# Performance work log

Hardware: AMD Instinct MI355X
Metric: run time of the kernel (lower is better)

The kernel has to match this reference:

```python
import jax, jax.numpy as jnp
import numpy as np

B, T, C = 4, 2048, 1024
H, DH = 16, 64  # num_heads, head_size; H*DH == C


def setup_inputs() -> dict:
    key = jax.random.key(0)
    ks = jax.random.split(key, 6)
    s = C ** -0.5
    x = jax.random.normal(ks[0], (B, T, C), dtype=jnp.float32)
    # per-head projection weights, stacked: [H, C, DH]
    Wq = jax.random.normal(ks[1], (H, C, DH), dtype=jnp.float32) * s
    Wk = jax.random.normal(ks[2], (H, C, DH), dtype=jnp.float32) * s
    Wv = jax.random.normal(ks[3], (H, C, DH), dtype=jnp.float32) * s
    # output projection (with bias, as nn.Linear default)
    Wo = jax.random.normal(ks[4], (C, C), dtype=jnp.float32) * s
    bo = jax.random.normal(ks[5], (C,), dtype=jnp.float32) * 0.01
    return {"x": x, "Wq": Wq, "Wk": Wk, "Wv": Wv, "Wo": Wo, "bo": bo}


def reference(x, Wq, Wk, Wv, Wo, bo):
    Bv, Tv, Cv = x.shape
    scale = DH ** -0.5
    # project to per-head q/k/v: [B, H, T, DH]
    q = jnp.einsum('btc,hcd->bhtd', x, Wq)
    k = jnp.einsum('btc,hcd->bhtd', x, Wk)
    v = jnp.einsum('btc,hcd->bhtd', x, Wv)
    # scaled scores [B, H, T, T] with causal mask
    scores = jnp.einsum('bhtd,bhsd->bhts', q, k) * scale
    causal = jnp.tril(jnp.ones((Tv, Tv), dtype=bool))
    scores = jnp.where(causal, scores, -jnp.inf)
    wei = jax.nn.softmax(scores, axis=-1)
    out = jnp.einsum('bhts,bhsd->bhtd', wei, v)
    # concat heads: [B, T, H*DH] == [B, T, C]
    out = out.transpose(0, 2, 1, 3).reshape(Bv, Tv, Cv)
    return out @ Wo.T + bo
```

## Files before the change

### kernel.cpp

```cpp
#include <hip/hip_runtime.h>
#include <stdint.h>

typedef unsigned short u16;
typedef __attribute__((ext_vector_type(8))) short short8;
typedef __attribute__((ext_vector_type(4))) float floatx4;

#define MFMA_BF16 __builtin_amdgcn_mfma_f32_16x16x32_bf16

#define BB 4
#define TT 2048
#define CC 1024
#define HH 16
#define DH 64
#define MM (BB * TT)
#define NQKV (3 * CC)

__device__ __forceinline__ u16 f2bf(float f) {
  union { float f; uint32_t u; } un;
  un.f = f;
  uint32_t u = un.u;
  u += 0x7fffu + ((u >> 16) & 1u);
  return (u16)(u >> 16);
}

__device__ __forceinline__ uint32_t pk2(float a, float b) {
  return (uint32_t)f2bf(a) | ((uint32_t)f2bf(b) << 16);
}

__device__ __forceinline__ uint32_t pktrunc(float a, float b) {
  union { float f; uint32_t u; } ua, ub;
  ua.f = a; ub.f = b;
  return __builtin_amdgcn_perm(ub.u, ua.u, 0x07060302u);
}

__device__ __forceinline__ void gload_lds16(const u16* g, u16* l) {
  __builtin_amdgcn_global_load_lds(
      (const __attribute__((address_space(1))) unsigned int*)g,
      (__attribute__((address_space(3))) unsigned int*)l, 16, 0, 0);
}

__global__ __launch_bounds__(256) void convert_kernel(
    const float* __restrict__ x, const float* __restrict__ Wq,
    const float* __restrict__ Wk, const float* __restrict__ Wv,
    const float* __restrict__ Wo, u16* __restrict__ xb,
    u16* __restrict__ Wt, u16* __restrict__ Wob) {
  __shared__ float T[32][33];
  int bid = blockIdx.x, tid = threadIdx.x;
  if (bid < 8192) {
    int i = (bid * 256 + tid) * 4;
    float4 f = *(const float4*)(x + i);
    uint2 o = {pk2(f.x, f.y), pk2(f.z, f.w)};
    *(uint2*)(xb + i) = o;
  } else if (bid < 8192 + 3072) {
    int tb = bid - 8192;
    int sec = tb >> 10, rem = tb & 1023;
    int h = rem >> 6, sub = rem & 63, ct = sub >> 1, dt = sub & 1;
    const float* W = (sec == 0) ? Wq : (sec == 1) ? Wk : Wv;
    int tx = tid & 31, ty = tid >> 5;
#pragma unroll
    for (int p = 0; p < 4; ++p)
      T[ty + 8 * p][tx] =
          W[((size_t)h * CC + ct * 32 + ty + 8 * p) * DH + dt * 32 + tx];
    __syncthreads();
#pragma unroll
    for (int p = 0; p < 4; ++p) {
      int n = sec * 1024 + h * 64 + dt * 32 + ty + 8 * p;
      Wt[(size_t)n * CC + ct * 32 + tx] = f2bf(T[tx][ty + 8 * p]);
    }
  } else {
    int i = ((bid - 11264) * 256 + tid) * 4;
    float4 f = *(const float4*)(Wo + i);
    uint2 o = {pk2(f.x, f.y), pk2(f.z, f.w)};
    *(uint2*)(Wob + i) = o;
  }
}

__global__ __launch_bounds__(512, 2) void gemm_qkv(
    const u16* __restrict__ A, const u16* __restrict__ Bt,
    u16* __restrict__ qout, u16* __restrict__ kout, u16* __restrict__ vout) {
  __shared__ u16 As[2 * 256 * 32];
  __shared__ u16 Bs[2 * 384 * 32];

  int tid = threadIdx.x;
  int lane = tid & 63, w = tid >> 6;
  int wr = w >> 2, wc = w & 3;
  int g = lane >> 4, c = lane & 15;
  int m0 = blockIdx.y * 256, n0 = blockIdx.x * 384;

  floatx4 acc[8][6];
#pragma unroll
  for (int i = 0; i < 8; ++i)
#pragma unroll
    for (int j = 0; j < 6; ++j) acc[i][j] = (floatx4){0.f, 0.f, 0.f, 0.f};

  int arow = tid >> 2, acol = (tid & 3) * 8;
  const u16* Ag = A + (size_t)(m0 + arow) * CC + acol;
  const u16* Bg = Bt + (size_t)(n0 + arow) * CC + acol;
  u16* asd = As + tid * 8;
  u16* bsd = Bs + tid * 8;

  const u16* Asr = As + (wr * 128 + c) * 32 + g * 8;
  const u16* Bsr = Bs + (wc * 96 + c) * 32 + g * 8;

  gload_lds16(Ag, asd);
  gload_lds16(Ag + (size_t)128 * CC, asd + 4096);
  gload_lds16(Bg, bsd);
  gload_lds16(Bg + (size_t)128 * CC, bsd + 4096);
  gload_lds16(Bg + (size_t)256 * CC, bsd + 8192);
  asm volatile("s_waitcnt vmcnt(0)" ::: "memory");
  __builtin_amdgcn_s_barrier();
  asm volatile("" ::: "memory");

#define GEMM_ITER(p, t)                                                       \
  {                                                                           \
    if ((t) + 1 < 32) {    \
      size_t ko = (size_t)((t) + 1) * 32;                                     \
      gload_lds16(Ag + ko, asd + ((p) ^ 1) * 8192);                           \
      gload_lds16(Ag + ko + (size_t)128 * CC, asd + ((p) ^ 1) * 8192 + 4096); \
      gload_lds16(Bg + ko, bsd + ((p) ^ 1) * 12288);                          \
      gload_lds16(Bg + ko + (size_t)128 * CC, bsd + ((p) ^ 1) * 12288 + 4096);\
      gload_lds16(Bg + ko + (size_t)256 * CC, bsd + ((p) ^ 1) * 12288 + 8192);\
    }                                                                         \
    short8 bfr[6];                                                            \
    _Pragma("unroll") for (int nt = 0; nt < 6; ++nt)                          \
        bfr[nt] = *(const short8*)(Bsr + (p) * 12288 + nt * 512);             \
    __builtin_amdgcn_s_setprio(1);                                            \
    _Pragma("unroll") for (int mt = 0; mt < 8; ++mt) {                        \
      short8 af = *(const short8*)(Asr + (p) * 8192 + mt * 512);              \
      _Pragma("unroll") for (int nt = 0; nt < 6; ++nt)                        \
          acc[mt][nt] = MFMA_BF16(af, bfr[nt], acc[mt][nt], 0, 0, 0);         \
    }                                                                         \
    __builtin_amdgcn_s_setprio(0);                                            \
    asm volatile("s_waitcnt vmcnt(0)" ::: "memory");    \
    __builtin_amdgcn_s_barrier();                                             \
    asm volatile("" ::: "memory");                                            \
  }

#pragma unroll 1
  for (int tt = 0; tt < 16; ++tt) {
    GEMM_ITER(0, 2 * tt);
    GEMM_ITER(1, 2 * tt + 1);
  }
#undef GEMM_ITER

  int mrow = m0 + wr * 128 + g * 4;
  int ncol = n0 + wc * 96 + c;
#pragma unroll
  for (int nt = 0; nt < 6; ++nt) {
    int n = ncol + nt * 16;
    int sec = n >> 10, h = (n >> 6) & 15, d = n & 63;
    u16* dst = (sec == 0) ? qout : (sec == 1) ? kout : vout;
    float sc = (sec == 0) ? 0.18033688011112042f : 1.f;
#pragma unroll
    for (int mt = 0; mt < 8; ++mt) {
#pragma unroll
      for (int r = 0; r < 4; ++r) {
        int m = mrow + mt * 16 + r;
        int b = m >> 11, t = m & 2047;
        dst[(((size_t)(b * HH + h)) * TT + t) * DH + d] =
            f2bf(acc[mt][nt][r] * sc);
      }
    }
  }
}

template <int MODE>
__global__ __launch_bounds__(256) void gemm_bt(
    const u16* __restrict__ A, const u16* __restrict__ Bt, int M, int N, int K,
    u16* __restrict__ qout, u16* __restrict__ kout, u16* __restrict__ vout,
    float* __restrict__ out, const float* __restrict__ bias) {
  __shared__ u16 As[128][64];
  __shared__ u16 Bs[128][64];
  int tid = threadIdx.x;
  int lane = tid & 63, w = tid >> 6;
  int wm = w >> 1, wn = w & 1;
  int g = lane >> 4, c = lane & 15;
  int m0 = blockIdx.y * 128, n0 = blockIdx.x * 128;

  floatx4 acc[4][4];
#pragma unroll
  for (int i = 0; i < 4; ++i)
#pragma unroll
    for (int j = 0; j < 4; ++j) acc[i][j] = (floatx4){0.f, 0.f, 0.f, 0.f};

  int srow = 32 * w + (lane >> 3);
  int scol = (lane & 7) * 8;
  const u16* Ag = A + (size_t)(m0 + srow) * K + scol;
  const u16* Bg = Bt + (size_t)(n0 + srow) * K + scol;
  u16* AsB = &As[32 * w][0];
  u16* BsB = &Bs[32 * w][0];

  for (int k0 = 0; k0 < K; k0 += 64) {
    __syncthreads();
#pragma unroll
    for (int j = 0; j < 4; ++j)
      gload_lds16(Ag + k0 + (size_t)j * 8 * K, AsB + j * 512);
#pragma unroll
    for (int j = 0; j < 4; ++j)
      gload_lds16(Bg + k0 + (size_t)j * 8 * K, BsB + j * 512);
    __syncthreads();
#pragma unroll
    for (int kc = 0; kc < 2; ++kc) {
      short8 af[4], bfv[4];
#pragma unroll
      for (int mt = 0; mt < 4; ++mt)
        af[mt] = *(const short8*)(&As[wm * 64 + mt * 16 + c][kc * 32 + g * 8]);
#pragma unroll
      for (int nt = 0; nt < 4; ++nt)
        bfv[nt] = *(const short8*)(&Bs[wn * 64 + nt * 16 + c][kc * 32 + g * 8]);
#pragma unroll
      for (int mt = 0; mt < 4; ++mt)
#pragma unroll
        for (int nt = 0; nt < 4; ++nt)
          acc[mt][nt] = MFMA_BF16(af[mt], bfv[nt], acc[mt][nt], 0, 0, 0);
    }
  }

#pragma unroll
  for (int mt = 0; mt < 4; ++mt) {
#pragma unroll
    for (int nt = 0; nt < 4; ++nt) {
#pragma unroll
      for (int r = 0; r < 4; ++r) {
        int m = m0 + wm * 64 + mt * 16 + g * 4 + r;
        int n = n0 + wn * 64 + nt * 16 + c;
        float v = acc[mt][nt][r];
        if (MODE == 0) {
          int b = m >> 11, t = m & 2047;
          int sec = n >> 10, h = (n >> 6) & 15, d = n & 63;
          size_t idx = (((size_t)(b * HH + h)) * TT + t) * DH + d;
          if (sec == 0)
            qout[idx] = f2bf(v * 0.18033688011112042f);
          else if (sec == 1)
            kout[idx] = f2bf(v);
          else
            vout[idx] = f2bf(v);
        } else {
          out[(size_t)m * N + n] = v + bias[n];
        }
      }
    }
  }
}

__global__ __launch_bounds__(256) void vtrans(const u16* __restrict__ v,
                                              u16* __restrict__ vP) {
  __shared__ u16 Ld[64][72];
  int tile = blockIdx.x, bh = blockIdx.y, tid = threadIdx.x;
  int row = tid >> 2, col = (tid & 3) * 16;
  const u16* src = v + ((size_t)bh * TT + tile * 64 + row) * DH + col;
  *(uint4*)(&Ld[row][col]) = *(const uint4*)(src);
  *(uint4*)(&Ld[row][col + 8]) = *(const uint4*)(src + 8);
  __syncthreads();
  int d = tid >> 2, u0 = (tid & 3) * 16;
  union { u16 h[16]; uint4 q[2]; } o;
#pragma unroll
  for (int k = 0; k < 16; ++k) {
    int u = u0 + k;
    int s = ((u & 3) << 4) | (u >> 2);
    o.h[k] = Ld[s][d];
  }
  u16* dst = vP + ((size_t)(bh * DH + d)) * TT + tile * 64 + u0;
  *(uint4*)(dst) = o.q[0];
  *(uint4*)(dst + 8) = o.q[1];
}

__constant__ unsigned char CHUNK_X[24] = {15, 15, 7, 14, 14, 13, 13, 6,
                                          12, 12, 11, 11, 5, 10, 10, 9,
                                          9,  4,  8,  8,  3, 2,  1,  0};
__constant__ unsigned char CHUNK_H[24] = {0, 1, 2, 0, 1, 0, 1, 2, 0, 1, 0, 1,
                                          2, 0, 1, 0, 1, 2, 0, 1, 2, 2, 2, 2};

__global__ __launch_bounds__(256, 4) void flash_attn(
    const u16* __restrict__ q, const u16* __restrict__ k,
    const u16* __restrict__ vP, u16* __restrict__ O,
    float* __restrict__ opart, float* __restrict__ lpart) {
  __shared__ u16 Ks[64][72];
  __shared__ u16 Vs[64][72];
  __shared__ u16 Ps[4][32][72];

  int tid = threadIdx.x;
  int lane = tid & 63, w = tid >> 6;
  int g = lane >> 4, c = lane & 15;

  int id = blockIdx.x;
  int e = id >> 6, bh = id & 63;
  int x = CHUNK_X[e], hf = CHUNK_H[e];
  int sb, se;
  if (hf == 2) {
    sb = 0; se = 2 * x + 2;
  } else {
    int n = x + 1; sb = hf * n; se = sb + n;
  }
  int t0 = x << 7;

  const u16* qb = q + (size_t)bh * TT * DH;
  const u16* kb = k + (size_t)bh * TT * DH;
  const u16* vb = vP + (size_t)bh * DH * TT;

  short8 qf[2][2];
#pragma unroll
  for (int mt = 0; mt < 2; ++mt) {
    int qrow = t0 + w * 32 + mt * 16 + c;
#pragma unroll
    for (int kc = 0; kc < 2; ++kc)
      qf[mt][kc] = *(const short8*)(qb + (size_t)qrow * DH + kc * 32 + g * 8);
  }

  const floatx4 zf = {0.f, 0.f, 0.f, 0.f};
  const short8 onesf = {(short)0x3F80, (short)0x3F80, (short)0x3F80,
                        (short)0x3F80, (short)0x3F80, (short)0x3F80,
                        (short)0x3F80, (short)0x3F80};

  floatx4 oacc[2][4];
#pragma unroll
  for (int mt = 0; mt < 2; ++mt)
#pragma unroll
    for (int nt = 0; nt < 4; ++nt) oacc[mt][nt] = zf;
  floatx4 lacc[2];
  lacc[0] = zf;
  lacc[1] = zf;

  int srow = tid >> 2, scol = (tid & 3) * 16;
  const u16* kbase = kb + (size_t)srow * DH + scol;
  const u16* vbase = vb + (size_t)srow * TT + scol;

  uint4 kr0 = *(const uint4*)(kbase + (size_t)(sb << 6) * DH);
  uint4 kr1 = *(const uint4*)(kbase + (size_t)(sb << 6) * DH + 8);
  uint4 vr0 = *(const uint4*)(vbase + (sb << 6));
  uint4 vr1 = *(const uint4*)(vbase + (sb << 6) + 8);

  int nfull = 2 * x;
  int wmax = t0 + w * 32 + 31;
  for (int it = sb; it < se; ++it) {
    int s0 = it << 6;
    __syncthreads();
    *(uint4*)(&Ks[srow][scol]) = kr0;
    *(uint4*)(&Ks[srow][scol + 8]) = kr1;
    *(uint4*)(&Vs[srow][scol]) = vr0;
    *(uint4*)(&Vs[srow][scol + 8]) = vr1;
    __syncthreads();
    if (it + 1 < se) {
      size_t koff = (size_t)((it + 1) << 6) * DH;
      int voff = (it + 1) << 6;
      kr0 = *(const uint4*)(kbase + koff);
      kr1 = *(const uint4*)(kbase + koff + 8);
      vr0 = *(const uint4*)(vbase + voff);
      vr1 = *(const uint4*)(vbase + voff + 8);
    }
    if (s0 > wmax) continue;
    bool masked = (it >= nfull);

    floatx4 z[2][4];
#pragma unroll
    for (int n = 0; n < 4; ++n) {
      short8 kf = *(const short8*)(&Ks[n * 16 + c][g * 8]);
      z[0][n] = MFMA_BF16(qf[0][0], kf, zf, 0, 0, 0);
      z[1][n] = MFMA_BF16(qf[1][0], kf, zf, 0, 0, 0);
    }
#pragma unroll
    for (int n = 0; n < 4; ++n) {
      short8 kf = *(const short8*)(&Ks[n * 16 + c][32 + g * 8]);
      z[0][n] = MFMA_BF16(qf[0][1], kf, z[0][n], 0, 0, 0);
      z[1][n] = MFMA_BF16(qf[1][1], kf, z[1][n], 0, 0, 0);
    }

#pragma unroll
    for (int mt = 0; mt < 2; ++mt) {
      int qr = t0 + w * 32 + mt * 16 + g * 4;
#pragma unroll
      for (int r = 0; r < 4; ++r) {
        float p0 = exp2f(z[mt][0][r]);
        float p1 = exp2f(z[mt][1][r]);
        float p2 = exp2f(z[mt][2][r]);
        float p3 = exp2f(z[mt][3][r]);
        if (masked) {
          if (s0 + c > qr + r) p0 = 0.f;
          if (s0 + 16 + c > qr + r) p1 = 0.f;
          if (s0 + 32 + c > qr + r) p2 = 0.f;
          if (s0 + 48 + c > qr + r) p3 = 0.f;
        }
        uint2 pk = {pktrunc(p0, p1), pktrunc(p2, p3)};
        *(uint2*)(&Ps[w][mt * 16 + g * 4 + r][4 * c]) = pk;
      }
    }

#pragma unroll
    for (int kc = 0; kc < 2; ++kc) {
      short8 pf0 = *(const short8*)(&Ps[w][c][kc * 32 + g * 8]);
      short8 pf1 = *(const short8*)(&Ps[w][16 + c][kc * 32 + g * 8]);
      lacc[0] = MFMA_BF16(pf0, onesf, lacc[0], 0, 0, 0);
      lacc[1] = MFMA_BF16(pf1, onesf, lacc[1], 0, 0, 0);
#pragma unroll
      for (int nt = 0; nt < 4; ++nt) {
        short8 vf = *(const short8*)(&Vs[nt * 16 + c][kc * 32 + g * 8]);
        oacc[0][nt] = MFMA_BF16(pf0, vf, oacc[0][nt], 0, 0, 0);
        oacc[1][nt] = MFMA_BF16(pf1, vf, oacc[1][nt], 0, 0, 0);
      }
    }
  }

  int b = bh >> 4, h = bh & 15;
  if (hf == 2) {
#pragma unroll
    for (int mt = 0; mt < 2; ++mt) {
      float inv[4];
#pragma unroll
      for (int r = 0; r < 4; ++r) inv[r] = 1.f / lacc[mt][r];
#pragma unroll
      for (int nt = 0; nt < 4; ++nt)
#pragma unroll
        for (int r = 0; r < 4; ++r) {
          int trow = t0 + w * 32 + mt * 16 + g * 4 + r;
          O[((size_t)b * TT + trow) * CC + h * DH + nt * 16 + c] =
              f2bf(oacc[mt][nt][r] * inv[r]);
        }
    }
  } else {
    float* os = opart + ((size_t)hf * 65536 + (size_t)bh * 1024) * 64;
    float* ls = lpart + (size_t)hf * 65536 + (size_t)bh * 1024;
#pragma unroll
    for (int mt = 0; mt < 2; ++mt) {
      int r0 = t0 - 1024 + w * 32 + mt * 16 + g * 4;
#pragma unroll
      for (int nt = 0; nt < 4; ++nt)
#pragma unroll
        for (int r = 0; r < 4; ++r)
          os[(size_t)(r0 + r) * 64 + nt * 16 + c] = oacc[mt][nt][r];
      if (c == 0)
#pragma unroll
        for (int r = 0; r < 4; ++r) ls[r0 + r] = lacc[mt][r];
    }
  }
}

__global__ __launch_bounds__(256) void merge_heavy(
    const float* __restrict__ op, const float* __restrict__ lp,
    u16* __restrict__ O) {
  int gid = blockIdx.x * 256 + threadIdx.x;
  int dq = gid & 15;
  int row = gid >> 4;
  float4 a = *(const float4*)(op + (size_t)row * 64 + dq * 4);
  float4 b = *(const float4*)(op + ((size_t)row + 65536) * 64 + dq * 4);
  float inv = 1.f / (lp[row] + lp[row + 65536]);
  int bh = row >> 10, lr = row & 1023;
  int bb = bh >> 4, h = bh & 15;
  u16* dst = O + ((size_t)bb * TT + 1024 + lr) * CC + h * DH + dq * 4;
  uint2 o = {pk2((a.x + b.x) * inv, (a.y + b.y) * inv),
             pk2((a.z + b.z) * inv, (a.w + b.w) * inv)};
  *(uint2*)dst = o;
}

extern "C" void kernel_launch(void* const* d_in, const int* in_sizes, int n_in,
                              void* d_out, int out_size, void* d_ws,
                              size_t ws_size, hipStream_t stream) {
  const float* x = (const float*)d_in[0];
  const float* Wq = (const float*)d_in[1];
  const float* Wk = (const float*)d_in[2];
  const float* Wv = (const float*)d_in[3];
  const float* Wo = (const float*)d_in[4];
  const float* bo = (const float*)d_in[5];
  float* out = (float*)d_out;

  u16* ws = (u16*)d_ws;
  u16* xb = ws;
  u16* Wt = xb + 8388608;
  u16* Wob = Wt + 3145728;
  u16* qw = Wob + 1048576;
  u16* kw = qw + 8388608;
  u16* vw = kw + 8388608;
  u16* vP = vw + 8388608;
  u16* Ow = xb;
  float* opart = (float*)d_out;
  float* lpart = (float*)Wt;

  convert_kernel<<<12288, 256, 0, stream>>>(x, Wq, Wk, Wv, Wo, xb, Wt, Wob);

  gemm_qkv<<<dim3(NQKV / 384, MM / 256), 512, 0, stream>>>(
      xb, Wt, qw, kw, vw);

  vtrans<<<dim3(TT / 64, BB * HH), 256, 0, stream>>>(vw, vP);

  flash_attn<<<dim3(1536), 256, 0, stream>>>(qw, kw, vP, Ow, opart, lpart);

  merge_heavy<<<dim3(4096), 256, 0, stream>>>(opart, lpart, Ow);

  gemm_bt<1><<<dim3(CC / 128, MM / 128), 256, 0, stream>>>(
      Ow, Wob, MM, CC, CC, nullptr, nullptr, nullptr, out, bo);
}
```

Measured before the change: 281.0 us.

## Restructure QKV GEMM into 128-row tiles with triple-buffered split-phase pipeline

```diff
diff --git a/kernel.cpp b/kernel.cpp
--- a/kernel.cpp
+++ b/kernel.cpp
@@ -37,6 +37,12 @@
   __builtin_amdgcn_global_load_lds(
       (const __attribute__((address_space(1))) unsigned int*)g,
       (__attribute__((address_space(3))) unsigned int*)l, 16, 0, 0);
+}
+
+__device__ __forceinline__ void BAR() {
+  asm volatile("" ::: "memory");
+  __builtin_amdgcn_s_barrier();
+  asm volatile("" ::: "memory");
 }
 
 __global__ __launch_bounds__(256) void convert_kernel(
@@ -78,18 +84,18 @@
 __global__ __launch_bounds__(512, 2) void gemm_qkv(
     const u16* __restrict__ A, const u16* __restrict__ Bt,
     u16* __restrict__ qout, u16* __restrict__ kout, u16* __restrict__ vout) {
-  __shared__ u16 As[2 * 256 * 32];
-  __shared__ u16 Bs[2 * 384 * 32];
+  __shared__ u16 As[3 * 128 * 32];
+  __shared__ u16 Bs[3 * 384 * 32];
 
   int tid = threadIdx.x;
   int lane = tid & 63, w = tid >> 6;
   int wr = w >> 2, wc = w & 3;
   int g = lane >> 4, c = lane & 15;
-  int m0 = blockIdx.y * 256, n0 = blockIdx.x * 384;
-
-  floatx4 acc[8][6];
-#pragma unroll
-  for (int i = 0; i < 8; ++i)
+  int m0 = blockIdx.y * 128, n0 = blockIdx.x * 384;
+
+  floatx4 acc[4][6];
+#pragma unroll
+  for (int i = 0; i < 4; ++i)
 #pragma unroll
     for (int j = 0; j < 6; ++j) acc[i][j] = (floatx4){0.f, 0.f, 0.f, 0.f};
 
@@ -99,51 +105,96 @@
   u16* asd = As + tid * 8;
   u16* bsd = Bs + tid * 8;
 
-  const u16* Asr = As + (wr * 128 + c) * 32 + g * 8;
-  const u16* Bsr = Bs + (wc * 96 + c) * 32 + g * 8;
+  int aro = (wr * 64 + c) * 32 + g * 8;
+  int bro = (wc * 96 + c) * 32 + g * 8;
 
   gload_lds16(Ag, asd);
-  gload_lds16(Ag + (size_t)128 * CC, asd + 4096);
   gload_lds16(Bg, bsd);
   gload_lds16(Bg + (size_t)128 * CC, bsd + 4096);
   gload_lds16(Bg + (size_t)256 * CC, bsd + 8192);
-  asm volatile("s_waitcnt vmcnt(0)" ::: "memory");
-  __builtin_amdgcn_s_barrier();
-  asm volatile("" ::: "memory");
-
-#define GEMM_ITER(p, t)                                                       \
+  gload_lds16(Ag + 32, asd + 4096);
+  gload_lds16(Bg + 32, bsd + 12288);
+  gload_lds16(Bg + 32 + (size_t)128 * CC, bsd + 12288 + 4096);
+  gload_lds16(Bg + 32 + (size_t)256 * CC, bsd + 12288 + 8192);
+  asm volatile("s_waitcnt vmcnt(4)" ::: "memory");
+  BAR();
+
+#define QTILE(SCA, SCB, SPA, SPB, T2, STG, VMW)                               \
   {                                                                           \
-    if ((t) + 1 < 32) {    \
-      size_t ko = (size_t)((t) + 1) * 32;                                     \
-      gload_lds16(Ag + ko, asd + ((p) ^ 1) * 8192);                           \
-      gload_lds16(Ag + ko + (size_t)128 * CC, asd + ((p) ^ 1) * 8192 + 4096); \
-      gload_lds16(Bg + ko, bsd + ((p) ^ 1) * 12288);                          \
-      gload_lds16(Bg + ko + (size_t)128 * CC, bsd + ((p) ^ 1) * 12288 + 4096);\
-      gload_lds16(Bg + ko + (size_t)256 * CC, bsd + ((p) ^ 1) * 12288 + 8192);\
+    short8 af0 = *(const short8*)(As + (SCA) + aro);                          \
+    short8 af1 = *(const short8*)(As + (SCA) + aro + 512);                    \
+    short8 af2 = *(const short8*)(As + (SCA) + aro + 1024);                   \
+    short8 af3 = *(const short8*)(As + (SCA) + aro + 1536);                   \
+    short8 bv0 = *(const short8*)(Bs + (SCB) + bro);                          \
+    short8 bv1 = *(const short8*)(Bs + (SCB) + bro + 512);                    \
+    short8 bv2 = *(const short8*)(Bs + (SCB) + bro + 1024);                   \
+    if (STG) {                                                                \
+      gload_lds16(Ag + (size_t)(T2) * 32, asd + (SPA));                       \
+      gload_lds16(Bg + (size_t)(T2) * 32, bsd + (SPB));                       \
     }                                                                         \
-    short8 bfr[6];                                                            \
-    _Pragma("unroll") for (int nt = 0; nt < 6; ++nt)                          \
-        bfr[nt] = *(const short8*)(Bsr + (p) * 12288 + nt * 512);             \
+    BAR();                                                                    \
     __builtin_amdgcn_s_setprio(1);                                            \
-    _Pragma("unroll") for (int mt = 0; mt < 8; ++mt) {                        \
-      short8 af = *(const short8*)(Asr + (p) * 8192 + mt * 512);              \
-      _Pragma("unroll") for (int nt = 0; nt < 6; ++nt)                        \
-          acc[mt][nt] = MFMA_BF16(af, bfr[nt], acc[mt][nt], 0, 0, 0);         \
+    acc[0][0] = MFMA_BF16(af0, bv0, acc[0][0], 0, 0, 0);                      \
+    acc[0][1] = MFMA_BF16(af0, bv1, acc[0][1], 0, 0, 0);                      \
+    acc[0][2] = MFMA_BF16(af0, bv2, acc[0][2], 0, 0, 0);                      \
+    acc[1][0] = MFMA_BF16(af1, bv0, acc[1][0], 0, 0, 0);                      \
+    acc[1][1] = MFMA_BF16(af1, bv1, acc[1][1], 0, 0, 0);                      \
+    acc[1][2] = MFMA_BF16(af1, bv2, acc[1][2], 0, 0, 0);                      \
+    acc[2][0] = MFMA_BF16(af2, bv0, acc[2][0], 0, 0, 0);                      \
+    acc[2][1] = MFMA_BF16(af2, bv1, acc[2][1], 0, 0, 0);                      \
+    acc[2][2] = MFMA_BF16(af2, bv2, acc[2][2], 0, 0, 0);                      \
+    acc[3][0] = MFMA_BF16(af3, bv0, acc[3][0], 0, 0, 0);                      \
+    acc[3][1] = MFMA_BF16(af3, bv1, acc[3][1], 0, 0, 0);                      \
+    acc[3][2] = MFMA_BF16(af3, bv2, acc[3][2], 0, 0, 0);                      \
+    __builtin_amdgcn_s_setprio(0);                                            \
+    BAR();                                                                    \
+    short8 bv3 = *(const short8*)(Bs + (SCB) + bro + 1536);                   \
+    short8 bv4 = *(const short8*)(Bs + (SCB) + bro + 2048);                   \
+    short8 bv5 = *(const short8*)(Bs + (SCB) + bro + 2560);                   \
+    if (STG) {                                                                \
+      gload_lds16(Bg + (size_t)(T2) * 32 + (size_t)128 * CC,                  \
+                  bsd + (SPB) + 4096);                                        \
+      gload_lds16(Bg + (size_t)(T2) * 32 + (size_t)256 * CC,                  \
+                  bsd + (SPB) + 8192);                                        \
     }                                                                         \
+    BAR();                                                                    \
+    __builtin_amdgcn_s_setprio(1);                                            \
+    acc[0][3] = MFMA_BF16(af0, bv3, acc[0][3], 0, 0, 0);                      \
+    acc[0][4] = MFMA_BF16(af0, bv4, acc[0][4], 0, 0, 0);                      \
+    acc[0][5] = MFMA_BF16(af0, bv5, acc[0][5], 0, 0, 0);                      \
+    acc[1][3] = MFMA_BF16(af1, bv3, acc[1][3], 0, 0, 0);                      \
+    acc[1][4] = MFMA_BF16(af1, bv4, acc[1][4], 0, 0, 0);                      \
+    acc[1][5] = MFMA_BF16(af1, bv5, acc[1][5], 0, 0, 0);                      \
+    acc[2][3] = MFMA_BF16(af2, bv3, acc[2][3], 0, 0, 0);                      \
+    acc[2][4] = MFMA_BF16(af2, bv4, acc[2][4], 0, 0, 0);                      \
+    acc[2][5] = MFMA_BF16(af2, bv5, acc[2][5], 0, 0, 0);                      \
+    acc[3][3] = MFMA_BF16(af3, bv3, acc[3][3], 0, 0, 0);                      \
+    acc[3][4] = MFMA_BF16(af3, bv4, acc[3][4], 0, 0, 0);                      \
+    acc[3][5] = MFMA_BF16(af3, bv5, acc[3][5], 0, 0, 0);                      \
     __builtin_amdgcn_s_setprio(0);                                            \
-    asm volatile("s_waitcnt vmcnt(0)" ::: "memory");    \
-    __builtin_amdgcn_s_barrier();                                             \
-    asm volatile("" ::: "memory");                                            \
-  }
-
+    VMW;                                                                      \
+    BAR();                                                                    \
+  }
+
+  int scA = 0, snA = 4096, spA = 8192;
+  int scB = 0, snB = 12288, spB = 24576;
 #pragma unroll 1
-  for (int tt = 0; tt < 16; ++tt) {
-    GEMM_ITER(0, 2 * tt);
-    GEMM_ITER(1, 2 * tt + 1);
-  }
-#undef GEMM_ITER
-
-  int mrow = m0 + wr * 128 + g * 4;
+  for (int t = 0; t < 30; ++t) {
+    QTILE(scA, scB, spA, spB, t + 2, 1,
+          asm volatile("s_waitcnt vmcnt(4)" ::: "memory"));
+    int ta = scA; scA = snA; snA = spA; spA = ta;
+    int tb = scB; scB = snB; snB = spB; spB = tb;
+  }
+  QTILE(scA, scB, spA, spB, 0, 0,
+        asm volatile("s_waitcnt vmcnt(0)" ::: "memory"));
+  {
+    int ta = scA; scA = snA; snA = spA; spA = ta;
+    int tb = scB; scB = snB; snB = spB; spB = tb;
+  }
+  QTILE(scA, scB, spA, spB, 0, 0, (void)0);
+#undef QTILE
+
+  int mrow = m0 + wr * 64 + g * 4;
   int ncol = n0 + wc * 96 + c;
 #pragma unroll
   for (int nt = 0; nt < 6; ++nt) {
@@ -152,7 +203,7 @@
     u16* dst = (sec == 0) ? qout : (sec == 1) ? kout : vout;
     float sc = (sec == 0) ? 0.18033688011112042f : 1.f;
 #pragma unroll
-    for (int mt = 0; mt < 8; ++mt) {
+    for (int mt = 0; mt < 4; ++mt) {
 #pragma unroll
       for (int r = 0; r < 4; ++r) {
         int m = mrow + mt * 16 + r;
@@ -476,7 +527,7 @@
 
   convert_kernel<<<12288, 256, 0, stream>>>(x, Wq, Wk, Wv, Wo, xb, Wt, Wob);
 
-  gemm_qkv<<<dim3(NQKV / 384, MM / 256), 512, 0, stream>>>(
+  gemm_qkv<<<dim3(NQKV / 384, MM / 128), 512, 0, stream>>>(
       xb, Wt, qw, kw, vw);
 
   vtrans<<<dim3(TT / 64, BB * HH), 256, 0, stream>>>(vw, vP);
```

After: 280.3 us. No clear change (-0.3%).
